# Performance work log

Measured on AMD Instinct MI355X. Metric: run time of the kernel, lower is better.

Reference implementation:

```python
import jax, jax.numpy as jnp
import numpy as np

B, S, D = 4, 4096, 2048
DFF = 4 * D
SKIP = 0.125


def setup_inputs() -> dict:
    key = jax.random.key(0)
    ks = jax.random.split(key, 4)
    s_in = 1.0 / np.sqrt(D).astype(np.float32)
    s_ff = 1.0 / np.sqrt(DFF).astype(np.float32)
    return {
        "x": jax.random.normal(ks[0], (B, S, D), jnp.float32),
        "Wr": jax.random.normal(ks[1], (D, 1), jnp.float32) * s_in,
        "br": jnp.zeros((1,), jnp.float32),
        "W1": jax.random.normal(ks[2], (D, DFF), jnp.float32) * s_in,
        "b1": jnp.zeros((DFF,), jnp.float32),
        "W2": jax.random.normal(ks[3], (DFF, D), jnp.float32) * s_ff,
        "b2": jnp.zeros((D,), jnp.float32),
    }


def reference(x, Wr, br, W1, b1, W2, b2):
    Bs, Ss, Ds = x.shape
    k = max(int(Ss * SKIP), 1)
    # Router: tiny linear D -> 1
    logits = (x @ Wr + br)[..., 0]                      # [B, S]
    # Top-k token selection along sequence
    weights, idx = jax.lax.top_k(logits, k)             # [B, k] (unsorted order within topk)
    perm = jnp.argsort(idx, axis=1)                     # torch.sort's sort-indices
    tokens = jnp.take_along_axis(idx, perm, axis=1)     # sorted token positions [B, k]
    # Gather selected tokens
    fx = jnp.take_along_axis(x, tokens[..., None], axis=1)  # [B, k, D]
    h = jax.nn.gelu(fx @ W1 + b1, approximate=False)    # [B, k, 4D]
    out_l = h @ W2 + b2                                  # [B, k, D]
    # Softmax over topk router logits, reordered to sorted-token order
    tw = jax.nn.softmax(weights, axis=1)                # [B, k]
    rw = jnp.take_along_axis(tw, perm, axis=1)          # [B, k]
    xw = rw[..., None] * out_l                           # [B, k, D]
    # scatter_add back onto x at the selected token positions
    bidx = jnp.arange(Bs)[:, None]                       # [B, 1]
    return x.at[bidx, tokens].add(xw)
```

## Files before the change

### kernel.cpp

```cpp
#include <hip/hip_runtime.h>
#include <math.h>

#define B_DIM   4
#define S_DIM   4096
#define D_DIM   2048
#define DFF_DIM 8192
#define K_TOP   512
#define M_ROWS  (B_DIM * K_TOP)
#define NSPLIT  4

typedef _Float16 half8 __attribute__((ext_vector_type(8)));
typedef _Float16 half4 __attribute__((ext_vector_type(4)));
typedef float    floatx4 __attribute__((ext_vector_type(4)));

static const size_t OFF_LOGITS = 0;
static const size_t OFF_SELMAP = 0;
static const size_t OFF_TOK    = 65536;
static const size_t OFF_RW     = 73728;
static const size_t OFF_FX     = 81920;
static const size_t OFF_W1T    = OFF_FX  + (size_t)M_ROWS * D_DIM * 2;
static const size_t OFF_W2T    = OFF_W1T + (size_t)DFF_DIM * D_DIM * 2;
static const size_t OFF_H      = OFF_W2T + (size_t)D_DIM * DFF_DIM * 2;
static const size_t WS_NEEDED  = OFF_H   + (size_t)M_ROWS * DFF_DIM * 2;
static const size_t OFF_PART   = OFF_W1T;

__device__ __forceinline__ void async_ld16(const void* g, void* l) {
  __builtin_amdgcn_global_load_lds((const __attribute__((address_space(1))) unsigned int*)g,
                                   (__attribute__((address_space(3))) unsigned int*)l,
                                   16, 0, 0);
}

#define WAITCNT_VM0   0x0F70

__global__ __launch_bounds__(256) void router_logits(const float* __restrict__ x,
                                                     const float* __restrict__ Wr,
                                                     const float* __restrict__ br,
                                                     float* __restrict__ logits) {
  int row  = blockIdx.x * 4 + (threadIdx.x >> 6);
  int lane = threadIdx.x & 63;
  const float4* xr = (const float4*)(x + (size_t)row * D_DIM);
  const float4* wr = (const float4*)Wr;
  float s = 0.f;
#pragma unroll
  for (int i = 0; i < (D_DIM / 4) / 64; ++i) {
    float4 a = xr[lane + i * 64];
    float4 w = wr[lane + i * 64];
    s += a.x * w.x + a.y * w.y + a.z * w.z + a.w * w.w;
  }
#pragma unroll
  for (int off = 32; off > 0; off >>= 1) s += __shfl_down(s, off, 64);
  if (lane == 0) logits[row] = s + br[0];
}

__global__ __launch_bounds__(256) void topk_select(const float* logits,
                                                   int* selmap,
                                                   int* __restrict__ tokens,
                                                   float* __restrict__ rw) {
  int b = blockIdx.x;
  const float* lg = logits + (size_t)b * S_DIM;
  __shared__ unsigned int keys[S_DIM];
  __shared__ unsigned int bins[256];
  __shared__ unsigned int sscan[256];
  __shared__ unsigned int sh_prefix, sh_r;
  __shared__ float sel_logit[K_TOP];
  __shared__ float red[8];

  int tid = threadIdx.x;
  for (int s = tid; s < S_DIM; s += 256) {
    unsigned int u = __float_as_uint(lg[s]);
    keys[s] = (u & 0x80000000u) ? ~u : (u | 0x80000000u);
    selmap[b * S_DIM + s] = -1;
  }
  if (tid == 0) { sh_prefix = 0u; sh_r = K_TOP; }
  __syncthreads();

  for (int p = 24; p >= 0; p -= 8) {
    bins[tid] = 0u;
    __syncthreads();
    unsigned int prefix = sh_prefix;
    unsigned int maskhi = (p == 24) ? 0u : (0xFFFFFFFFu << (p + 8));
    for (int s = tid; s < S_DIM; s += 256) {
      unsigned int kk = keys[s];
      if ((kk & maskhi) == prefix) atomicAdd(&bins[(kk >> p) & 255u], 1u);
    }
    __syncthreads();
    sscan[tid] = bins[255 - tid];
    __syncthreads();
#pragma unroll
    for (int off = 1; off < 256; off <<= 1) {
      unsigned int v = (tid >= off) ? sscan[tid - off] : 0u;
      __syncthreads();
      sscan[tid] += v;
      __syncthreads();
    }
    unsigned int r = sh_r;
    unsigned int above = (tid > 0) ? sscan[tid - 1] : 0u;
    bool hit = (sscan[tid] >= r) && (above < r);
    __syncthreads();
    if (hit) {
      sh_prefix = prefix | ((unsigned int)(255 - tid) << p);
      sh_r = r - above;
    }
    __syncthreads();
  }
  unsigned int T = sh_prefix;

  int s0 = tid * 16;
  unsigned int g = 0, e = 0;
#pragma unroll
  for (int j = 0; j < 16; ++j) {
    unsigned int kk = keys[s0 + j];
    g += (kk > T);
    e += (kk == T);
  }
  sscan[tid] = g | (e << 16);
  __syncthreads();
#pragma unroll
  for (int off = 1; off < 256; off <<= 1) {
    unsigned int v = (tid >= off) ? sscan[tid - off] : 0u;
    __syncthreads();
    sscan[tid] += v;
    __syncthreads();
  }
  unsigned int incl = sscan[tid];
  unsigned int Gtot = sscan[255] & 0xFFFFu;
  unsigned int need = (unsigned int)K_TOP - Gtot;
  unsigned int gr = (incl & 0xFFFFu) - g;
  unsigned int er = (incl >> 16) - e;
#pragma unroll
  for (int j = 0; j < 16; ++j) {
    unsigned int kk = keys[s0 + j];
    if (kk > T) {
      unsigned int pos = gr + (er < need ? er : need);
      tokens[b * K_TOP + (int)pos] = s0 + j;
      sel_logit[pos] = __uint_as_float((kk & 0x80000000u) ? (kk & 0x7FFFFFFFu) : ~kk);
      selmap[b * S_DIM + s0 + j] = (int)pos;
      gr++;
    } else if (kk == T) {
      if (er < need) {
        unsigned int pos = gr + er;
        tokens[b * K_TOP + (int)pos] = s0 + j;
        sel_logit[pos] = __uint_as_float((kk & 0x80000000u) ? (kk & 0x7FFFFFFFu) : ~kk);
        selmap[b * S_DIM + s0 + j] = (int)pos;
      }
      er++;
    }
  }
  __syncthreads();

  int lane = tid & 63, wv = tid >> 6;
  float mx = -1e30f;
  for (int i = tid; i < K_TOP; i += 256) mx = fmaxf(mx, sel_logit[i]);
#pragma unroll
  for (int off = 32; off > 0; off >>= 1) mx = fmaxf(mx, __shfl_down(mx, off, 64));
  if (lane == 0) red[wv] = mx;
  __syncthreads();
  if (tid == 0) red[0] = fmaxf(fmaxf(red[0], red[1]), fmaxf(red[2], red[3]));
  __syncthreads();
  float M = red[0];
  float sm = 0.f;
  for (int i = tid; i < K_TOP; i += 256) sm += expf(sel_logit[i] - M);
#pragma unroll
  for (int off = 32; off > 0; off >>= 1) sm += __shfl_down(sm, off, 64);
  if (lane == 0) red[4 + wv] = sm;
  __syncthreads();
  if (tid == 0) red[4] = red[4] + red[5] + red[6] + red[7];
  __syncthreads();
  float SUM = red[4];
  for (int i = tid; i < K_TOP; i += 256) rw[b * K_TOP + i] = expf(sel_logit[i] - M) / SUM;
}

__global__ __launch_bounds__(256) void transpose_cvt(const float* __restrict__ in,
                                                     _Float16* __restrict__ out,
                                                     int K, int N) {
  __shared__ float tile[64][65];
  int nb = blockIdx.x * 64, kb = blockIdx.y * 64;
  int tid = threadIdx.x;
  int lr = tid >> 4;
  int lc = (tid & 15) * 4;
#pragma unroll
  for (int p = 0; p < 4; ++p) {
    int row = p * 16 + lr;
    float4 v = *(const float4*)(in + (size_t)(kb + row) * N + nb + lc);
    tile[row][lc] = v.x; tile[row][lc + 1] = v.y; tile[row][lc + 2] = v.z; tile[row][lc + 3] = v.w;
  }
  __syncthreads();
#pragma unroll
  for (int p = 0; p < 2; ++p) {
    int cc = p * 256 + tid;
    int n  = cc >> 3;
    int kc = (cc & 7) * 8;
    half8 o;
#pragma unroll
    for (int j = 0; j < 8; ++j) o[j] = (_Float16)tile[kc + j][n];
    *(half8*)(out + (size_t)(nb + n) * K + kb + kc) = o;
  }
}

__global__ __launch_bounds__(256) void gather_cvt(const float* __restrict__ x,
                                                  const int* __restrict__ tokens,
                                                  _Float16* __restrict__ fx) {
  int row = blockIdx.x;
  int b = row >> 9;
  int token = tokens[row];
  const float4* src = (const float4*)(x + ((size_t)b * S_DIM + token) * D_DIM);
  half4* dst = (half4*)(fx + (size_t)row * D_DIM);
  for (int i = threadIdx.x; i < D_DIM / 4; i += 256) {
    float4 v = src[i];
    half4 o;
    o[0] = (_Float16)v.x; o[1] = (_Float16)v.y; o[2] = (_Float16)v.z; o[3] = (_Float16)v.w;
    dst[i] = o;
  }
}

#define MFMA_CLUSTER(ACCBASE, AF, BF)                                                   \
  __builtin_amdgcn_s_setprio(1);                                                        \
  _Pragma("unroll")                                                                     \
  for (int i_ = 0; i_ < 4; ++i_)                                                        \
    _Pragma("unroll")                                                                   \
    for (int j_ = 0; j_ < 4; ++j_)                                                      \
      acc[(ACCBASE) + i_][j_] =                                                         \
          __builtin_amdgcn_mfma_f32_16x16x32_f16(AF[i_], BF[j_], acc[(ACCBASE) + i_][j_], 0, 0, 0); \
  __builtin_amdgcn_s_setprio(0);

template <int EPI>
__global__ __launch_bounds__(512, 2) void gemm256(const _Float16* __restrict__ A,
                                                  const _Float16* __restrict__ Bt,
                                                  const float* __restrict__ bias,
                                                  _Float16* __restrict__ Co,
                                                  int M, int N, int K, int Kspan) {
  __shared__ _Float16 As[2][256 * 64];
  __shared__ _Float16 Bs[2][256 * 64];
  const int tid  = threadIdx.x;
  const int lane = tid & 63;
  const int wave = __builtin_amdgcn_readfirstlane(tid >> 6);
  const int wm   = wave >> 2;
  const int wn   = wave & 3;

  const int nwg = gridDim.x * gridDim.y;
  const int bid = blockIdx.y * gridDim.x + blockIdx.x;
  const int swb = (bid & 7) * (nwg >> 3) + (bid >> 3);
  const int bn  = (swb % gridDim.x) * 256;
  const int bm  = (swb / gridDim.x) * 256;

  const int k0 = blockIdx.z * Kspan;
  const int nt = Kspan / 64;

  const int lr  = lane >> 3;
  const int lcs = ((lane & 7) ^ lr) * 8;
  const _Float16* a_lane = A  + (size_t)(bm + lr) * K + k0 + lcs;
  const _Float16* b_lane = Bt + (size_t)(bn + lr) * K + k0 + lcs;
  size_t goff[2][2];
  int    ldso[2][2];
#pragma unroll
  for (int h = 0; h < 2; ++h)
#pragma unroll
    for (int ci = 0; ci < 2; ++ci) {
      const int cip = 2 * wave + ci;
      goff[h][ci] = (size_t)(h * 128 + cip * 8) * K;
      ldso[h][ci] = h * 8192 + cip * 512;
    }

  const int mr   = lane & 15;
  const int ksub = lane >> 4;
  const int xr   = mr & 7;
  const int sc0  = (ksub ^ xr) * 8;
  const int sc1  = ((ksub ^ xr) ^ 4) * 8;
  const int aro  = (wm * 128 + mr) * 64;
  const int bro  = (wn * 64 + mr) * 64;

  floatx4 acc[8][4] = {};
  half8 af_a[4], af_b[4], bf_a[4], bf_b[4];

#pragma unroll
  for (int h = 0; h < 2; ++h)
#pragma unroll
    for (int ci = 0; ci < 2; ++ci) {
      async_ld16(a_lane + goff[h][ci], &As[0][ldso[h][ci]]);
      async_ld16(b_lane + goff[h][ci], &Bs[0][ldso[h][ci]]);
    }
  __builtin_amdgcn_s_waitcnt(WAITCNT_VM0);
  __builtin_amdgcn_s_barrier();
  __builtin_amdgcn_sched_barrier(0);
#pragma unroll
  for (int i = 0; i < 4; ++i) af_a[i] = *(const half8*)(&As[0][aro + i * 1024 + sc0]);
#pragma unroll
  for (int j = 0; j < 4; ++j) bf_a[j] = *(const half8*)(&Bs[0][bro + j * 1024 + sc0]);

  for (int t = 0; t < nt; ++t) {
    const _Float16* as = As[t & 1];
    const _Float16* bs = Bs[t & 1];

    if (t + 1 < nt) {
      const int kt = (t + 1) * 64;
      _Float16* an = &As[(t + 1) & 1][0];
      _Float16* bn2 = &Bs[(t + 1) & 1][0];
#pragma unroll
      for (int h = 0; h < 2; ++h)
#pragma unroll
        for (int ci = 0; ci < 2; ++ci) {
          async_ld16(a_lane + goff[h][ci] + kt, an + ldso[h][ci]);
          async_ld16(b_lane + goff[h][ci] + kt, bn2 + ldso[h][ci]);
        }
    }
#pragma unroll
    for (int i = 0; i < 4; ++i) af_b[i] = *(const half8*)(as + aro + 4096 + i * 1024 + sc0);
    __builtin_amdgcn_sched_barrier(0);
    MFMA_CLUSTER(0, af_a, bf_a)
    __builtin_amdgcn_s_barrier();

#pragma unroll
    for (int i = 0; i < 4; ++i) af_a[i] = *(const half8*)(as + aro + i * 1024 + sc1);
#pragma unroll
    for (int j = 0; j < 4; ++j) bf_b[j] = *(const half8*)(bs + bro + j * 1024 + sc1);
    __builtin_amdgcn_sched_barrier(0);
    MFMA_CLUSTER(4, af_b, bf_a)
    __builtin_amdgcn_s_barrier();

#pragma unroll
    for (int i = 0; i < 4; ++i) af_b[i] = *(const half8*)(as + aro + 4096 + i * 1024 + sc1);
    __builtin_amdgcn_sched_barrier(0);
    MFMA_CLUSTER(0, af_a, bf_b)
    __builtin_amdgcn_s_barrier();

    __builtin_amdgcn_s_waitcnt(WAITCNT_VM0);
    __builtin_amdgcn_s_barrier();
    __builtin_amdgcn_sched_barrier(0);
    if (t + 1 < nt) {
      const _Float16* asn = As[(t + 1) & 1];
      const _Float16* bsn = Bs[(t + 1) & 1];
#pragma unroll
      for (int i = 0; i < 4; ++i) af_a[i] = *(const half8*)(asn + aro + i * 1024 + sc0);
#pragma unroll
      for (int j = 0; j < 4; ++j) bf_a[j] = *(const half8*)(bsn + bro + j * 1024 + sc0);
    }
    __builtin_amdgcn_sched_barrier(0);
    MFMA_CLUSTER(4, af_b, bf_b)
    __builtin_amdgcn_s_barrier();
  }

  const int r0 = (lane >> 4) * 4;
  const int cn = lane & 15;
  if (EPI == 0) {
#pragma unroll
    for (int i = 0; i < 8; ++i) {
      const int row = bm + wm * 128 + (i >> 2) * 64 + (i & 3) * 16 + r0;
#pragma unroll
      for (int j = 0; j < 4; ++j) {
        const int col = bn + wn * 64 + j * 16 + cn;
        const float bv = bias[col];
#pragma unroll
        for (int r = 0; r < 4; ++r) {
          float v = acc[i][j][r] + bv;
          v = 0.5f * v * (1.0f + erff(v * 0.7071067811865475f));
          Co[(size_t)(row + r) * N + col] = (_Float16)v;
        }
      }
    }
  } else {
    const size_t zoff = (size_t)blockIdx.z * M;
#pragma unroll
    for (int i = 0; i < 8; ++i) {
      const int row = bm + wm * 128 + (i >> 2) * 64 + (i & 3) * 16 + r0;
#pragma unroll
      for (int j = 0; j < 4; ++j) {
        const int col = bn + wn * 64 + j * 16 + cn;
#pragma unroll
        for (int r = 0; r < 4; ++r)
          Co[(zoff + row + r) * N + col] = (_Float16)acc[i][j][r];
      }
    }
  }
}

__global__ __launch_bounds__(256) void finalize(const float* __restrict__ x,
                                                const _Float16* __restrict__ part,
                                                const float* __restrict__ bias,
                                                const int* __restrict__ selmap,
                                                const float* __restrict__ rw,
                                                float* __restrict__ out) {
  int row = blockIdx.x;
  size_t base = (size_t)row * D_DIM;
  int sel = selmap[row];
  int c = threadIdx.x * 8;
  float4 o0 = *(const float4*)(x + base + c);
  float4 o1 = *(const float4*)(x + base + c + 4);
  if (sel >= 0) {
    float wgt = rw[sel];
    float acc[8] = {0, 0, 0, 0, 0, 0, 0, 0};
#pragma unroll
    for (int kz = 0; kz < NSPLIT; ++kz) {
      half8 p = *(const half8*)(part + ((size_t)kz * M_ROWS + sel) * D_DIM + c);
#pragma unroll
      for (int j = 0; j < 8; ++j) acc[j] += (float)p[j];
    }
    float4 b0 = *(const float4*)(bias + c);
    float4 b1 = *(const float4*)(bias + c + 4);
    o0.x += wgt * (acc[0] + b0.x);
    o0.y += wgt * (acc[1] + b0.y);
    o0.z += wgt * (acc[2] + b0.z);
    o0.w += wgt * (acc[3] + b0.w);
    o1.x += wgt * (acc[4] + b1.x);
    o1.y += wgt * (acc[5] + b1.y);
    o1.z += wgt * (acc[6] + b1.z);
    o1.w += wgt * (acc[7] + b1.w);
  }
  *(float4*)(out + base + c)     = o0;
  *(float4*)(out + base + c + 4) = o1;
}

extern "C" void kernel_launch(void* const* d_in, const int* in_sizes, int n_in,
                              void* d_out, int out_size, void* d_ws, size_t ws_size,
                              hipStream_t stream) {
  const float* x  = (const float*)d_in[0];
  const float* Wr = (const float*)d_in[1];
  const float* br = (const float*)d_in[2];
  const float* W1 = (const float*)d_in[3];
  const float* b1 = (const float*)d_in[4];
  const float* W2 = (const float*)d_in[5];
  const float* b2 = (const float*)d_in[6];
  float* out = (float*)d_out;

  if (ws_size < WS_NEEDED) return;

  char* ws = (char*)d_ws;
  float*     logits = (float*)(ws + OFF_LOGITS);
  int*       selmap = (int*)(ws + OFF_SELMAP);
  int*       tokens = (int*)(ws + OFF_TOK);
  float*     rw     = (float*)(ws + OFF_RW);
  _Float16*  fx     = (_Float16*)(ws + OFF_FX);
  _Float16*  W1T    = (_Float16*)(ws + OFF_W1T);
  _Float16*  W2T    = (_Float16*)(ws + OFF_W2T);
  _Float16*  h      = (_Float16*)(ws + OFF_H);
  _Float16*  part   = (_Float16*)(ws + OFF_PART);

  transpose_cvt<<<dim3(DFF_DIM / 64, D_DIM / 64), 256, 0, stream>>>(W1, W1T, D_DIM, DFF_DIM);
  transpose_cvt<<<dim3(D_DIM / 64, DFF_DIM / 64), 256, 0, stream>>>(W2, W2T, DFF_DIM, D_DIM);

  router_logits<<<(B_DIM * S_DIM) / 4, 256, 0, stream>>>(x, Wr, br, logits);
  topk_select<<<B_DIM, 256, 0, stream>>>(logits, selmap, tokens, rw);
  gather_cvt<<<M_ROWS, 256, 0, stream>>>(x, tokens, fx);

  gemm256<0><<<dim3(DFF_DIM / 256, M_ROWS / 256, 1), 512, 0, stream>>>(
      fx, W1T, b1, h, M_ROWS, DFF_DIM, D_DIM, D_DIM);
  gemm256<2><<<dim3(D_DIM / 256, M_ROWS / 256, NSPLIT), 512, 0, stream>>>(
      h, W2T, nullptr, part, M_ROWS, D_DIM, DFF_DIM, DFF_DIM / NSPLIT);
  finalize<<<B_DIM * S_DIM, 256, 0, stream>>>(x, part, b2, selmap, rw, out);
}
```

Baseline: 579.8 us.

## Restructure GEMM LDS layout into k-halves and interleave async loads with MFMA phases

Reorganizes the shared-memory tile layout so each 64-wide k tile is stored as two 32-wide halves with a new XOR swizzle. The next tile's global-to-LDS loads are split into four groups issued between the MFMA clusters, and partial vmcnt waits let half of the next tile land while compute continues. Fragment registers drop from four sets to two, which reduces register pressure. The cost is more barriers per iteration, and the waitcnt encodings and the new swizzle must be right for the results to stay correct.

```diff
diff --git a/kernel.cpp b/kernel.cpp
--- a/kernel.cpp
+++ b/kernel.cpp
@@ -30,7 +30,9 @@
                                    16, 0, 0);
 }
 
+#define WAITCNT_VM4   0x0F74
 #define WAITCNT_VM0   0x0F70
+#define WAITCNT_LGKM0 0xC07F
 
 __global__ __launch_bounds__(256) void router_logits(const float* __restrict__ x,
                                                      const float* __restrict__ Wr,
@@ -229,8 +231,8 @@
                                                   const float* __restrict__ bias,
                                                   _Float16* __restrict__ Co,
                                                   int M, int N, int K, int Kspan) {
-  __shared__ _Float16 As[2][256 * 64];
-  __shared__ _Float16 Bs[2][256 * 64];
+  __shared__ _Float16 As[2][16384];
+  __shared__ _Float16 Bs[2][16384];
   const int tid  = threadIdx.x;
   const int lane = tid & 63;
   const int wave = __builtin_amdgcn_readfirstlane(tid >> 6);
@@ -246,97 +248,100 @@
   const int k0 = blockIdx.z * Kspan;
   const int nt = Kspan / 64;
 
-  const int lr  = lane >> 3;
-  const int lcs = ((lane & 7) ^ lr) * 8;
-  const _Float16* a_lane = A  + (size_t)(bm + lr) * K + k0 + lcs;
-  const _Float16* b_lane = Bt + (size_t)(bn + lr) * K + k0 + lcs;
-  size_t goff[2][2];
-  int    ldso[2][2];
-#pragma unroll
-  for (int h = 0; h < 2; ++h)
-#pragma unroll
-    for (int ci = 0; ci < 2; ++ci) {
-      const int cip = 2 * wave + ci;
-      goff[h][ci] = (size_t)(h * 128 + cip * 8) * K;
-      ldso[h][ci] = h * 8192 + cip * 512;
-    }
+  const int l4   = lane >> 2;
+  const int jsel = (lane & 3) ^ ((lane >> 3) & 3);
+  const _Float16* aw = A  + (size_t)(bm + wave * 32 + l4) * K + k0;
+  const _Float16* bw = Bt + (size_t)(bn + wave * 32 + l4) * K + k0;
+  const int c0 = jsel * 8;
+  const int c1 = (4 + jsel) * 8;
+  const int d0 = wave * 1024;
+  const size_t rstep = (size_t)16 * K;
 
   const int mr   = lane & 15;
   const int ksub = lane >> 4;
-  const int xr   = mr & 7;
-  const int sc0  = (ksub ^ xr) * 8;
-  const int sc1  = ((ksub ^ xr) ^ 4) * 8;
-  const int aro  = (wm * 128 + mr) * 64;
-  const int bro  = (wn * 64 + mr) * 64;
+  const int sc   = (ksub ^ ((mr >> 1) & 3)) * 8;
+  const int aro  = (wm * 128 + mr) * 32 + sc;
+  const int bro  = (wn * 64 + mr) * 32 + sc;
 
   floatx4 acc[8][4] = {};
-  half8 af_a[4], af_b[4], bf_a[4], bf_b[4];
-
-#pragma unroll
-  for (int h = 0; h < 2; ++h)
-#pragma unroll
-    for (int ci = 0; ci < 2; ++ci) {
-      async_ld16(a_lane + goff[h][ci], &As[0][ldso[h][ci]]);
-      async_ld16(b_lane + goff[h][ci], &Bs[0][ldso[h][ci]]);
-    }
+  half8 af[4], bf[4];
+
+#pragma unroll
+  for (int u = 0; u < 2; ++u) async_ld16(aw + u * rstep + c0, &As[0][d0 + u * 512]);
+#pragma unroll
+  for (int u = 0; u < 2; ++u) async_ld16(bw + u * rstep + c0, &Bs[0][d0 + u * 512]);
+#pragma unroll
+  for (int u = 0; u < 2; ++u) async_ld16(aw + u * rstep + c1, &As[0][8192 + d0 + u * 512]);
+#pragma unroll
+  for (int u = 0; u < 2; ++u) async_ld16(bw + u * rstep + c1, &Bs[0][8192 + d0 + u * 512]);
   __builtin_amdgcn_s_waitcnt(WAITCNT_VM0);
   __builtin_amdgcn_s_barrier();
   __builtin_amdgcn_sched_barrier(0);
-#pragma unroll
-  for (int i = 0; i < 4; ++i) af_a[i] = *(const half8*)(&As[0][aro + i * 1024 + sc0]);
-#pragma unroll
-  for (int j = 0; j < 4; ++j) bf_a[j] = *(const half8*)(&Bs[0][bro + j * 1024 + sc0]);
 
   for (int t = 0; t < nt; ++t) {
     const _Float16* as = As[t & 1];
     const _Float16* bs = Bs[t & 1];
-
-    if (t + 1 < nt) {
-      const int kt = (t + 1) * 64;
-      _Float16* an = &As[(t + 1) & 1][0];
-      _Float16* bn2 = &Bs[(t + 1) & 1][0];
-#pragma unroll
-      for (int h = 0; h < 2; ++h)
-#pragma unroll
-        for (int ci = 0; ci < 2; ++ci) {
-          async_ld16(a_lane + goff[h][ci] + kt, an + ldso[h][ci]);
-          async_ld16(b_lane + goff[h][ci] + kt, bn2 + ldso[h][ci]);
-        }
-    }
-#pragma unroll
-    for (int i = 0; i < 4; ++i) af_b[i] = *(const half8*)(as + aro + 4096 + i * 1024 + sc0);
-    __builtin_amdgcn_sched_barrier(0);
-    MFMA_CLUSTER(0, af_a, bf_a)
-    __builtin_amdgcn_s_barrier();
-
-#pragma unroll
-    for (int i = 0; i < 4; ++i) af_a[i] = *(const half8*)(as + aro + i * 1024 + sc1);
-#pragma unroll
-    for (int j = 0; j < 4; ++j) bf_b[j] = *(const half8*)(bs + bro + j * 1024 + sc1);
-    __builtin_amdgcn_sched_barrier(0);
-    MFMA_CLUSTER(4, af_b, bf_a)
-    __builtin_amdgcn_s_barrier();
-
-#pragma unroll
-    for (int i = 0; i < 4; ++i) af_b[i] = *(const half8*)(as + aro + 4096 + i * 1024 + sc1);
-    __builtin_amdgcn_sched_barrier(0);
-    MFMA_CLUSTER(0, af_a, bf_b)
-    __builtin_amdgcn_s_barrier();
-
-    __builtin_amdgcn_s_waitcnt(WAITCNT_VM0);
-    __builtin_amdgcn_s_barrier();
-    __builtin_amdgcn_sched_barrier(0);
-    if (t + 1 < nt) {
-      const _Float16* asn = As[(t + 1) & 1];
-      const _Float16* bsn = Bs[(t + 1) & 1];
-#pragma unroll
-      for (int i = 0; i < 4; ++i) af_a[i] = *(const half8*)(asn + aro + i * 1024 + sc0);
-#pragma unroll
-      for (int j = 0; j < 4; ++j) bf_a[j] = *(const half8*)(bsn + bro + j * 1024 + sc0);
-    }
-    __builtin_amdgcn_sched_barrier(0);
-    MFMA_CLUSTER(4, af_b, bf_b)
-    __builtin_amdgcn_s_barrier();
+    _Float16* nxA = &As[(t + 1) & 1][0];
+    _Float16* nxB = &Bs[(t + 1) & 1][0];
+    const bool more = (t + 1 < nt);
+    const int kt = (t + 1) * 64;
+
+#pragma unroll
+    for (int i = 0; i < 4; ++i) af[i] = *(const half8*)(as + aro + i * 512);
+#pragma unroll
+    for (int j = 0; j < 4; ++j) bf[j] = *(const half8*)(bs + bro + j * 512);
+    if (more) {
+      async_ld16(aw + kt + c0, nxA + d0);
+      async_ld16(aw + rstep + kt + c0, nxA + d0 + 512);
+    }
+    __builtin_amdgcn_s_barrier();
+    __builtin_amdgcn_s_waitcnt(WAITCNT_LGKM0);
+    __builtin_amdgcn_sched_barrier(0);
+    MFMA_CLUSTER(0, af, bf)
+    __builtin_amdgcn_s_barrier();
+
+#pragma unroll
+    for (int i = 0; i < 4; ++i) af[i] = *(const half8*)(as + 2048 + aro + i * 512);
+    if (more) {
+      async_ld16(bw + kt + c0, nxB + d0);
+      async_ld16(bw + rstep + kt + c0, nxB + d0 + 512);
+    }
+    __builtin_amdgcn_s_barrier();
+    __builtin_amdgcn_s_waitcnt(WAITCNT_LGKM0);
+    __builtin_amdgcn_sched_barrier(0);
+    MFMA_CLUSTER(4, af, bf)
+    if (more) __builtin_amdgcn_s_waitcnt(WAITCNT_VM4);
+    else      __builtin_amdgcn_s_waitcnt(WAITCNT_VM0);
+    __builtin_amdgcn_s_barrier();
+    __builtin_amdgcn_sched_barrier(0);
+
+#pragma unroll
+    for (int i = 0; i < 4; ++i) af[i] = *(const half8*)(as + 8192 + aro + i * 512);
+#pragma unroll
+    for (int j = 0; j < 4; ++j) bf[j] = *(const half8*)(bs + 8192 + bro + j * 512);
+    if (more) {
+      async_ld16(aw + kt + c1, nxA + 8192 + d0);
+      async_ld16(aw + rstep + kt + c1, nxA + 8192 + d0 + 512);
+    }
+    __builtin_amdgcn_s_barrier();
+    __builtin_amdgcn_s_waitcnt(WAITCNT_LGKM0);
+    __builtin_amdgcn_sched_barrier(0);
+    MFMA_CLUSTER(0, af, bf)
+    __builtin_amdgcn_s_barrier();
+
+#pragma unroll
+    for (int i = 0; i < 4; ++i) af[i] = *(const half8*)(as + 8192 + 2048 + aro + i * 512);
+    if (more) {
+      async_ld16(bw + kt + c1, nxB + 8192 + d0);
+      async_ld16(bw + rstep + kt + c1, nxB + 8192 + d0 + 512);
+    }
+    __builtin_amdgcn_s_barrier();
+    __builtin_amdgcn_s_waitcnt(WAITCNT_LGKM0);
+    __builtin_amdgcn_sched_barrier(0);
+    MFMA_CLUSTER(4, af, bf)
+    if (more) __builtin_amdgcn_s_waitcnt(WAITCNT_VM4);
+    __builtin_amdgcn_s_barrier();
+    __builtin_amdgcn_sched_barrier(0);
   }
 
   const int r0 = (lane >> 4) * 4;
```

Result: no change. 587.9 us (+1.4%).
